# Optimization experiments

Measured on AMD Instinct MI355X. Metric: run time of the kernel, lower is better.

## Reference

```python
import jax, jax.numpy as jnp
import numpy as np

NUM_HEADS = 16
HEAD_DIM = 64
D_MODEL = 1024
OUTPUT_DIM = 1024


def setup_inputs() -> dict:
    key = jax.random.key(0)
    ks = jax.random.split(key, 11)
    B, S, H = 2, 2048, D_MODEL
    inner = NUM_HEADS * HEAD_DIM
    s = 0.02
    return {
        "query": jax.random.normal(ks[0], (B, S, H), jnp.float32),
        "key": jax.random.normal(ks[1], (B, S, H), jnp.float32),
        "value": jax.random.normal(ks[2], (B, S, H), jnp.float32),
        "Wq": jax.random.normal(ks[3], (H, inner), jnp.float32) * s,
        "bq": jnp.zeros((inner,), jnp.float32),
        "Wk": jax.random.normal(ks[4], (H, inner), jnp.float32) * s,
        "bk": jnp.zeros((inner,), jnp.float32),
        "Wv": jax.random.normal(ks[5], (H, inner), jnp.float32) * s,
        "bv": jnp.zeros((inner,), jnp.float32),
        "Wo": jax.random.normal(ks[6], (inner, OUTPUT_DIM), jnp.float32) * s,
        "bo": jnp.zeros((OUTPUT_DIM,), jnp.float32),
    }


def reference(query, key, value, Wq, bq, Wk, bk, Wv, bv, Wo, bo):
    B, Sq, _ = query.shape
    Sk = key.shape[1]
    nh, dh = NUM_HEADS, HEAD_DIM
    # projections -> [B, S, nh, dh]
    Q = (query @ Wq + bq).reshape(B, Sq, nh, dh)
    K = (key @ Wk + bk).reshape(B, Sk, nh, dh)
    V = (value @ Wv + bv).reshape(B, Sk, nh, dh)
    # scores [B, nh, Sq, Sk]
    scores = jnp.einsum("bqhd,bkhd->bhqk", Q, K) / jnp.sqrt(jnp.float32(dh))
    attn = jax.nn.softmax(scores, axis=-1)
    out = jnp.einsum("bhqk,bkhd->bqhd", attn, V).reshape(B, Sq, nh * dh)
    return out @ Wo + bo
```

## Files before the change

### kernel.cpp

```cpp
#include <hip/hip_runtime.h>
#include <math.h>

typedef __attribute__((ext_vector_type(8))) short short8;
typedef __attribute__((ext_vector_type(4))) short short4v;
typedef __attribute__((ext_vector_type(4))) float f32x4;
typedef __attribute__((ext_vector_type(2))) float f32x2;

#if __has_builtin(__builtin_amdgcn_mfma_f32_16x16x16bf16_1k)
#define HAVE_MFMA16 1
#else
#define HAVE_MFMA16 0
#endif

__device__ __forceinline__ short f2bf(float f) {
  union { float f; unsigned u; } x; x.f = f;
  unsigned r = x.u + 0x7fffu + ((x.u >> 16) & 1u);
  return (short)(r >> 16);
}
__device__ __forceinline__ unsigned pack_bf(float a, float b) {
  union { float f; unsigned u; } x, y; x.f = a; y.f = b;
  unsigned ra = x.u + 0x7fffu + ((x.u >> 16) & 1u);
  unsigned rb = y.u + 0x7fffu + ((y.u >> 16) & 1u);
  return (ra >> 16) | (rb & 0xffff0000u);
}
union U4S8 { unsigned u[4]; short8 s; };
union U2S4 { unsigned u[2]; short4v s; };

template <bool A_IS_F32, bool OUT_F32, int BM>
__global__ __launch_bounds__(256) void gemm_bias(
    const void* __restrict__ A0, const void* __restrict__ A1, const void* __restrict__ A2,
    const float* __restrict__ B0, const float* __restrict__ B1, const float* __restrict__ B2,
    const float* __restrict__ b0, const float* __restrict__ b1, const float* __restrict__ b2,
    void* __restrict__ C0, void* __restrict__ C1, void* __restrict__ C2,
    int M, int N, int K) {
  const int z = blockIdx.z;
  const void*  Av   = z == 0 ? A0 : (z == 1 ? A1 : A2);
  const float* B    = z == 0 ? B0 : (z == 1 ? B1 : B2);
  const float* bias = z == 0 ? b0 : (z == 1 ? b1 : b2);
  void*        Cv   = z == 0 ? C0 : (z == 1 ? C1 : C2);

  constexpr int MF = BM / 32;
  __shared__ __align__(16) short As[BM * 40];
  __shared__ __align__(16) short Bs[128 * 40];
  const int tid = threadIdx.x;
  const int l = tid & 63, w = tid >> 6;
  const int lr = l & 15, lq = l >> 4;
  const int lin = blockIdx.x + (int)gridDim.x * blockIdx.y;
  const int ny = (int)gridDim.y;
  const int yb = lin % ny, xb = lin / ny;
  const int m0 = yb * BM, n0 = xb * 128;
  const int wm = (w >> 1) * (BM / 2), wn = (w & 1) * 64;
  f32x4 acc[MF][4] = {};

  constexpr int TPR = 256 / BM;
  const int ar = tid / TPR, ac = (tid % TPR) * (32 / TPR);
  const int dp = tid & 63, kb = tid >> 6;

  f32x4 avf[MF];
  short8 avb[MF / 2];
  f32x2 bvf[8];

  auto load_regs = [&](int k0) {
    if constexpr (A_IS_F32) {
      const float* Ap = (const float*)Av + (size_t)(m0 + ar) * K + k0 + ac;
#pragma unroll
      for (int i = 0; i < MF; ++i) avf[i] = *(const f32x4*)(Ap + 4 * i);
    } else {
      const short* Ap = (const short*)Av + (size_t)(m0 + ar) * K + k0 + ac;
#pragma unroll
      for (int i = 0; i < MF / 2; ++i) avb[i] = *(const short8*)(Ap + 8 * i);
    }
    const float* Bp = B + (size_t)(k0 + kb * 8) * N + n0 + 2 * dp;
#pragma unroll
    for (int i = 0; i < 4; ++i) {
      bvf[2 * i]     = *(const f32x2*)(Bp + (size_t)(2 * i) * N);
      bvf[2 * i + 1] = *(const f32x2*)(Bp + (size_t)(2 * i + 1) * N);
    }
  };
  auto write_lds = [&]() {
    if constexpr (A_IS_F32) {
#pragma unroll
      for (int j = 0; j < MF / 2; ++j) {
        U4S8 p;
        p.u[0] = pack_bf(avf[2 * j][0], avf[2 * j][1]);
        p.u[1] = pack_bf(avf[2 * j][2], avf[2 * j][3]);
        p.u[2] = pack_bf(avf[2 * j + 1][0], avf[2 * j + 1][1]);
        p.u[3] = pack_bf(avf[2 * j + 1][2], avf[2 * j + 1][3]);
        *(short8*)&As[ar * 40 + ac + 8 * j] = p.s;
      }
    } else {
#pragma unroll
      for (int j = 0; j < MF / 2; ++j)
        *(short8*)&As[ar * 40 + ac + 8 * j] = avb[j];
    }
    U4S8 lo, hi;
#pragma unroll
    for (int i = 0; i < 4; ++i) {
      lo.u[i] = pack_bf(bvf[2 * i][0], bvf[2 * i + 1][0]);
      hi.u[i] = pack_bf(bvf[2 * i][1], bvf[2 * i + 1][1]);
    }
    *(short8*)&Bs[(2 * dp) * 40 + kb * 8] = lo.s;
    *(short8*)&Bs[(2 * dp + 1) * 40 + kb * 8] = hi.s;
  };

  load_regs(0);
  const int KT = K >> 5;
  for (int kt = 0; kt < KT; ++kt) {
    write_lds();
    __syncthreads();
    if (kt + 1 < KT) load_regs((kt + 1) * 32);

    short8 af[MF], bfr[4];
#pragma unroll
    for (int i = 0; i < MF; ++i)
      af[i] = *(const short8*)&As[(wm + i * 16 + lr) * 40 + lq * 8];
#pragma unroll
    for (int i = 0; i < 4; ++i)
      bfr[i] = *(const short8*)&Bs[(wn + i * 16 + lr) * 40 + lq * 8];
#pragma unroll
    for (int mi = 0; mi < MF; ++mi)
#pragma unroll
      for (int ni = 0; ni < 4; ++ni)
        acc[mi][ni] = __builtin_amdgcn_mfma_f32_16x16x32_bf16(af[mi], bfr[ni], acc[mi][ni], 0, 0, 0);
    __syncthreads();
  }

#pragma unroll
  for (int ni = 0; ni < 4; ++ni) {
    int gn = n0 + wn + ni * 16 + lr;
    float bv = bias[gn];
#pragma unroll
    for (int mi = 0; mi < MF; ++mi) {
      int gm = m0 + wm + mi * 16 + lq * 4;
#pragma unroll
      for (int r = 0; r < 4; ++r) {
        float val = acc[mi][ni][r] + bv;
        if constexpr (OUT_F32)
          ((float*)Cv)[(size_t)(gm + r) * N + gn] = val;
        else
          ((short*)Cv)[(size_t)(gm + r) * N + gn] = f2bf(val);
      }
    }
  }
}

__global__ __launch_bounds__(256) void attn128(
    const short* __restrict__ Q, const short* __restrict__ K,
    const short* __restrict__ V, short* __restrict__ ctx) {
  __shared__ __align__(16) short Ks[64][72];
  __shared__ __align__(16) short Vt[64][72];
#if !HAVE_MFMA16
  __shared__ __align__(16) short Ps2[4][32][68];
#endif
  const int tid = threadIdx.x, l = tid & 63, w = tid >> 6;
  const int lr = l & 15, lq = l >> 4;
  const int lin = blockIdx.x + 16 * blockIdx.y;
  const int h = lin & 15, qblk = lin >> 4;
  const int b = blockIdx.z, q0 = qblk * 128;
  const size_t bh = (size_t)b * 2048 * 1024 + (size_t)h * 64;
  const short* Kg = K + bh;
  const short* Vg = V + bh;

  short8 qb[2][2];
#pragma unroll
  for (int qf = 0; qf < 2; ++qf)
#pragma unroll
    for (int ks = 0; ks < 2; ++ks)
      qb[qf][ks] = *(const short8*)&Q[bh + (size_t)(q0 + w * 32 + qf * 16 + lr) * 1024 + ks * 32 + lq * 8];

  f32x4 accO[4][2] = {};
  float lpart[2] = {0.f, 0.f};

  const int kr = tid >> 2, kc = (tid & 3) * 16;
  const int vdp = tid & 31, vkb = tid >> 5;

  short8 kv0, kv1;
  unsigned vu[8];
  auto load_kv = [&](int kt) {
    const short* Kp = &Kg[(size_t)(kt * 64 + kr) * 1024 + kc];
    kv0 = *(const short8*)(Kp + 0);
    kv1 = *(const short8*)(Kp + 8);
#pragma unroll
    for (int i = 0; i < 8; ++i)
      vu[i] = *(const unsigned*)&Vg[(size_t)(kt * 64 + vkb * 8 + i) * 1024 + vdp * 2];
  };
  auto write_kv = [&]() {
    *(short8*)&Ks[kr][kc] = kv0;
    *(short8*)&Ks[kr][kc + 8] = kv1;
    U4S8 lo, hi;
#pragma unroll
    for (int j = 0; j < 4; ++j) {
      lo.u[j] = (vu[2 * j] & 0xffffu) | (vu[2 * j + 1] << 16);
      hi.u[j] = (vu[2 * j] >> 16) | (vu[2 * j + 1] & 0xffff0000u);
    }
    *(short8*)&Vt[2 * vdp][vkb * 8] = lo.s;
    *(short8*)&Vt[2 * vdp + 1][vkb * 8] = hi.s;
  };

  load_kv(0);
  for (int kt = 0; kt < 32; ++kt) {
    write_kv();
    __syncthreads();
    if (kt + 1 < 32) load_kv(kt + 1);

    short8 ka[4][2];
#pragma unroll
    for (int ni = 0; ni < 4; ++ni)
#pragma unroll
      for (int ks = 0; ks < 2; ++ks)
        ka[ni][ks] = *(const short8*)&Ks[ni * 16 + lr][ks * 32 + lq * 8];
    f32x4 s[4][2] = {};
#pragma unroll
    for (int ni = 0; ni < 4; ++ni)
#pragma unroll
      for (int qf = 0; qf < 2; ++qf) {
        s[ni][qf] = __builtin_amdgcn_mfma_f32_16x16x32_bf16(ka[ni][0], qb[qf][0], s[ni][qf], 0, 0, 0);
        s[ni][qf] = __builtin_amdgcn_mfma_f32_16x16x32_bf16(ka[ni][1], qb[qf][1], s[ni][qf], 0, 0, 0);
      }

    unsigned pk[4][2][2];
#pragma unroll
    for (int ni = 0; ni < 4; ++ni)
#pragma unroll
      for (int qf = 0; qf < 2; ++qf) {
        float p0 = __expf(s[ni][qf][0] * 0.125f);
        float p1 = __expf(s[ni][qf][1] * 0.125f);
        float p2 = __expf(s[ni][qf][2] * 0.125f);
        float p3 = __expf(s[ni][qf][3] * 0.125f);
        lpart[qf] += (p0 + p1) + (p2 + p3);
        pk[ni][qf][0] = pack_bf(p0, p1);
        pk[ni][qf][1] = pack_bf(p2, p3);
      }

#if HAVE_MFMA16
#pragma unroll
    for (int di = 0; di < 4; ++di)
#pragma unroll
      for (int ni = 0; ni < 4; ++ni) {
        short4v vb = *(const short4v*)&Vt[di * 16 + lr][ni * 16 + lq * 4];
#pragma unroll
        for (int qf = 0; qf < 2; ++qf) {
          U2S4 a; a.u[0] = pk[ni][qf][0]; a.u[1] = pk[ni][qf][1];
          accO[di][qf] = __builtin_amdgcn_mfma_f32_16x16x16bf16_1k(a.s, vb, accO[di][qf], 0, 0, 0);
        }
      }
#else
#pragma unroll
    for (int ni = 0; ni < 4; ++ni)
#pragma unroll
      for (int qf = 0; qf < 2; ++qf) {
        unsigned* dst = (unsigned*)&Ps2[w][qf * 16 + lr][16 * ni + 4 * lq];
        dst[0] = pk[ni][qf][0];
        dst[1] = pk[ni][qf][1];
      }
#pragma unroll
    for (int ks = 0; ks < 2; ++ks)
#pragma unroll
      for (int qf = 0; qf < 2; ++qf) {
        const short* src = &Ps2[w][qf * 16 + lr][32 * ks + 8 * lq];
        U4S8 a;
        a.u[0] = ((const unsigned*)src)[0]; a.u[1] = ((const unsigned*)src)[1];
        a.u[2] = ((const unsigned*)src)[2]; a.u[3] = ((const unsigned*)src)[3];
#pragma unroll
        for (int di = 0; di < 4; ++di) {
          short8 vb = *(const short8*)&Vt[di * 16 + lr][ks * 32 + lq * 8];
          accO[di][qf] = __builtin_amdgcn_mfma_f32_16x16x32_bf16(a.s, vb, accO[di][qf], 0, 0, 0);
        }
      }
#endif
    __syncthreads();
  }

#pragma unroll
  for (int qf = 0; qf < 2; ++qf) {
    lpart[qf] += __shfl_xor(lpart[qf], 16, 64);
    lpart[qf] += __shfl_xor(lpart[qf], 32, 64);
  }
  float inv[2] = {1.0f / lpart[0], 1.0f / lpart[1]};
  float ir[2][4];
#pragma unroll
  for (int qf = 0; qf < 2; ++qf)
#pragma unroll
    for (int r = 0; r < 4; ++r)
      ir[qf][r] = __shfl(inv[qf], 4 * lq + r, 64);

#pragma unroll
  for (int qf = 0; qf < 2; ++qf)
#pragma unroll
    for (int r = 0; r < 4; ++r) {
      size_t row = bh + (size_t)(q0 + w * 32 + qf * 16 + 4 * lq + r) * 1024;
#pragma unroll
      for (int di = 0; di < 4; ++di)
        ctx[row + di * 16 + lr] = f2bf(accO[di][qf][r] * ir[qf][r]);
    }
}

extern "C" void kernel_launch(void* const* d_in, const int* in_sizes, int n_in,
                              void* d_out, int out_size, void* d_ws, size_t ws_size,
                              hipStream_t stream) {
  const void*  query = d_in[0];
  const void*  key   = d_in[1];
  const void*  value = d_in[2];
  const float* Wq = (const float*)d_in[3];
  const float* bq = (const float*)d_in[4];
  const float* Wk = (const float*)d_in[5];
  const float* bk = (const float*)d_in[6];
  const float* Wv = (const float*)d_in[7];
  const float* bv = (const float*)d_in[8];
  const float* Wo = (const float*)d_in[9];
  const float* bo = (const float*)d_in[10];

  short* ws = (short*)d_ws;
  const size_t MT = 4096ull * 1024ull;
  short* Qb = ws;
  short* Vb = ws + MT;
  short* Kb = (short*)d_out;

  gemm_bias<true, false, 64><<<dim3(8, 64, 3), 256, 0, stream>>>(
      query, key, value, Wq, Wk, Wv, bq, bk, bv, Qb, Kb, Vb, 4096, 1024, 1024);
  attn128<<<dim3(16, 16, 2), 256, 0, stream>>>(Qb, Kb, Vb, Qb );
  gemm_bias<false, true, 64><<<dim3(8, 64, 1), 256, 0, stream>>>(
      Qb, Qb, Qb, Wo, Wo, Wo, bo, bo, bo, d_out, d_out, d_out, 4096, 1024, 1024);
}
```

Before: 282.9 us.

## Pre-transpose weights to bf16 and use BM=128 tiles for QKV projection

Adds a kernel that converts the fp32 weight matrices to bf16 in transposed (N-major) layout, so the GEMMs load B tiles as contiguous bf16 vectors with no per-tile conversion. The QKV projection also switches to BM=128 tiles, halving the grid's row blocks. This adds an extra launch and extra weight traffic on every call, and it relies on workspace size, falling back to storing transposed weights in the output buffer's tail.

```diff
diff --git a/kernel.cpp b/kernel.cpp
--- a/kernel.cpp
+++ b/kernel.cpp
@@ -26,16 +26,52 @@
 union U4S8 { unsigned u[4]; short8 s; };
 union U2S4 { unsigned u[2]; short4v s; };
 
-template <bool A_IS_F32, bool OUT_F32, int BM>
+__global__ __launch_bounds__(256) void wconv(
+    const float* __restrict__ W0, const float* __restrict__ W1,
+    const float* __restrict__ W2, const float* __restrict__ W3,
+    short* __restrict__ T0, short* __restrict__ T1,
+    short* __restrict__ T2, short* __restrict__ T3) {
+  const float* W; short* T;
+  switch (blockIdx.z) {
+    case 0: W = W0; T = T0; break;
+    case 1: W = W1; T = T1; break;
+    case 2: W = W2; T = T2; break;
+    default: W = W3; T = T3; break;
+  }
+  __shared__ __align__(16) short t[64][72];
+  const int tid = threadIdx.x;
+  const int x0 = blockIdx.x * 64, y0 = blockIdx.y * 64;
+  {
+    int rr = tid >> 2, cc = (tid & 3) * 16;
+    const float* p = W + (size_t)(x0 + rr) * 1024 + y0 + cc;
+    f32x4 v[4];
+    v[0] = *(const f32x4*)(p + 0);  v[1] = *(const f32x4*)(p + 4);
+    v[2] = *(const f32x4*)(p + 8);  v[3] = *(const f32x4*)(p + 12);
+#pragma unroll
+    for (int i = 0; i < 4; ++i)
+#pragma unroll
+      for (int j = 0; j < 4; ++j)
+        t[cc + 4 * i + j][rr] = f2bf(v[i][j]);
+  }
+  __syncthreads();
+  {
+    int nr = tid >> 2, kc = (tid & 3) * 16;
+    short* q = T + (size_t)(y0 + nr) * 1024 + x0 + kc;
+    *(short8*)q       = *(const short8*)&t[nr][kc];
+    *(short8*)(q + 8) = *(const short8*)&t[nr][kc + 8];
+  }
+}
+
+template <bool A_IS_F32, bool B_IS_BF16, bool OUT_F32, int BM>
 __global__ __launch_bounds__(256) void gemm_bias(
     const void* __restrict__ A0, const void* __restrict__ A1, const void* __restrict__ A2,
-    const float* __restrict__ B0, const float* __restrict__ B1, const float* __restrict__ B2,
+    const void* __restrict__ B0, const void* __restrict__ B1, const void* __restrict__ B2,
     const float* __restrict__ b0, const float* __restrict__ b1, const float* __restrict__ b2,
     void* __restrict__ C0, void* __restrict__ C1, void* __restrict__ C2,
     int M, int N, int K) {
   const int z = blockIdx.z;
   const void*  Av   = z == 0 ? A0 : (z == 1 ? A1 : A2);
-  const float* B    = z == 0 ? B0 : (z == 1 ? B1 : B2);
+  const void*  Bv   = z == 0 ? B0 : (z == 1 ? B1 : B2);
   const float* bias = z == 0 ? b0 : (z == 1 ? b1 : b2);
   void*        Cv   = z == 0 ? C0 : (z == 1 ? C1 : C2);
 
@@ -54,10 +90,12 @@
 
   constexpr int TPR = 256 / BM;
   const int ar = tid / TPR, ac = (tid % TPR) * (32 / TPR);
+  const int br = tid >> 1, bcc = (tid & 1) * 16;
   const int dp = tid & 63, kb = tid >> 6;
 
   f32x4 avf[MF];
-  short8 avb[MF / 2];
+  short8 avb[BM / 64 > 0 ? BM / 64 : 1];
+  short8 bvb[2];
   f32x2 bvf[8];
 
   auto load_regs = [&](int k0) {
@@ -68,13 +106,19 @@
     } else {
       const short* Ap = (const short*)Av + (size_t)(m0 + ar) * K + k0 + ac;
 #pragma unroll
-      for (int i = 0; i < MF / 2; ++i) avb[i] = *(const short8*)(Ap + 8 * i);
-    }
-    const float* Bp = B + (size_t)(k0 + kb * 8) * N + n0 + 2 * dp;
-#pragma unroll
-    for (int i = 0; i < 4; ++i) {
-      bvf[2 * i]     = *(const f32x2*)(Bp + (size_t)(2 * i) * N);
-      bvf[2 * i + 1] = *(const f32x2*)(Bp + (size_t)(2 * i + 1) * N);
+      for (int i = 0; i < BM / 64; ++i) avb[i] = *(const short8*)(Ap + 8 * i);
+    }
+    if constexpr (B_IS_BF16) {
+      const short* Bp = (const short*)Bv + (size_t)(n0 + br) * K + k0 + bcc;
+      bvb[0] = *(const short8*)(Bp + 0);
+      bvb[1] = *(const short8*)(Bp + 8);
+    } else {
+      const float* Bp = (const float*)Bv + (size_t)(k0 + kb * 8) * N + n0 + 2 * dp;
+#pragma unroll
+      for (int i = 0; i < 4; ++i) {
+        bvf[2 * i]     = *(const f32x2*)(Bp + (size_t)(2 * i) * N);
+        bvf[2 * i + 1] = *(const f32x2*)(Bp + (size_t)(2 * i + 1) * N);
+      }
     }
   };
   auto write_lds = [&]() {
@@ -90,17 +134,22 @@
       }
     } else {
 #pragma unroll
-      for (int j = 0; j < MF / 2; ++j)
+      for (int j = 0; j < BM / 64; ++j)
         *(short8*)&As[ar * 40 + ac + 8 * j] = avb[j];
     }
-    U4S8 lo, hi;
-#pragma unroll
-    for (int i = 0; i < 4; ++i) {
-      lo.u[i] = pack_bf(bvf[2 * i][0], bvf[2 * i + 1][0]);
-      hi.u[i] = pack_bf(bvf[2 * i][1], bvf[2 * i + 1][1]);
-    }
-    *(short8*)&Bs[(2 * dp) * 40 + kb * 8] = lo.s;
-    *(short8*)&Bs[(2 * dp + 1) * 40 + kb * 8] = hi.s;
+    if constexpr (B_IS_BF16) {
+      *(short8*)&Bs[br * 40 + bcc] = bvb[0];
+      *(short8*)&Bs[br * 40 + bcc + 8] = bvb[1];
+    } else {
+      U4S8 lo, hi;
+#pragma unroll
+      for (int i = 0; i < 4; ++i) {
+        lo.u[i] = pack_bf(bvf[2 * i][0], bvf[2 * i + 1][0]);
+        hi.u[i] = pack_bf(bvf[2 * i][1], bvf[2 * i + 1][1]);
+      }
+      *(short8*)&Bs[(2 * dp) * 40 + kb * 8] = lo.s;
+      *(short8*)&Bs[(2 * dp + 1) * 40 + kb * 8] = hi.s;
+    }
   };
 
   load_regs(0);
@@ -312,13 +361,33 @@
 
   short* ws = (short*)d_ws;
   const size_t MT = 4096ull * 1024ull;
+  const size_t WSZ = 1024ull * 1024ull;
   short* Qb = ws;
   short* Vb = ws + MT;
   short* Kb = (short*)d_out;
 
-  gemm_bias<true, false, 64><<<dim3(8, 64, 3), 256, 0, stream>>>(
-      query, key, value, Wq, Wk, Wv, bq, bk, bv, Qb, Kb, Vb, 4096, 1024, 1024);
+  const bool roomy = ws_size >= (2 * MT + 4 * WSZ) * sizeof(short);
+  short *WqT, *WkT, *WvT, *WoT;
+  if (roomy) {
+    short* base = ws + 2 * MT;
+    WqT = base; WkT = base + WSZ; WvT = base + 2 * WSZ; WoT = base + 3 * WSZ;
+  } else {
+    short* tail = (short*)d_out + MT;
+    WqT = tail; WkT = tail + WSZ; WvT = tail + 2 * WSZ; WoT = nullptr;
+  }
+
+  wconv<<<dim3(16, 16, roomy ? 4 : 3), 256, 0, stream>>>(
+      Wq, Wk, Wv, Wo, WqT, WkT, WvT, roomy ? WoT : WvT);
+
+  gemm_bias<true, true, false, 128><<<dim3(8, 32, 3), 256, 0, stream>>>(
+      query, key, value, WqT, WkT, WvT, bq, bk, bv, Qb, Kb, Vb, 4096, 1024, 1024);
+
   attn128<<<dim3(16, 16, 2), 256, 0, stream>>>(Qb, Kb, Vb, Qb );
-  gemm_bias<false, true, 64><<<dim3(8, 64, 1), 256, 0, stream>>>(
-      Qb, Qb, Qb, Wo, Wo, Wo, bo, bo, bo, d_out, d_out, d_out, 4096, 1024, 1024);
-}
+
+  if (roomy)
+    gemm_bias<false, true, true, 64><<<dim3(8, 64, 1), 256, 0, stream>>>(
+        Qb, Qb, Qb, WoT, WoT, WoT, bo, bo, bo, d_out, d_out, d_out, 4096, 1024, 1024);
+  else
+    gemm_bias<false, false, true, 64><<<dim3(8, 64, 1), 256, 0, stream>>>(
+        Qb, Qb, Qb, Wo, Wo, Wo, bo, bo, bo, d_out, d_out, d_out, 4096, 1024, 1024);
+}
```

Measured after the change: 266.1 us. 1.06x faster.
